# Kernel optimization log

Hardware: AMD Instinct MI355X
Metric: run time of the kernel (lower is better)

## Reference

```python
import jax, jax.numpy as jnp
import numpy as np
from jax import lax

STRIDE = 4
NSAMPLE = 16
EPS = 1e-5


def farthest_point_sample(xyz, npoint):
    # xyz: [B, N, 3] -> indices [B, npoint]. Deterministic start at index 0.
    B, N, _ = xyz.shape
    def step(carry, _):
        distance, farthest = carry
        centroid = jnp.take_along_axis(xyz, farthest[:, None, None], axis=1)  # [B,1,3]
        dist = jnp.sum((xyz - centroid) ** 2, axis=-1)  # [B,N]
        distance = jnp.minimum(distance, dist)
        new_farthest = jnp.argmax(distance, axis=-1).astype(jnp.int32)
        return (distance, new_farthest), farthest
    init = (jnp.full((B, N), 1e10, dtype=xyz.dtype), jnp.zeros((B,), dtype=jnp.int32))
    _, cents = lax.scan(step, init, None, length=npoint)  # [npoint, B]
    return cents.T  # [B, npoint]


def index_points(points, idx):
    # points: [B, N, C], idx: [B, ...] -> [B, ..., C]
    B = points.shape[0]
    C = points.shape[-1]
    flat = idx.reshape(B, -1)
    out = jnp.take_along_axis(points, flat[..., None], axis=1)
    return out.reshape(*idx.shape, C)


def square_distance(src, dst):
    # src: [B,N,3], dst: [B,M,3] -> [B,N,M]
    d = -2.0 * jnp.einsum('bnc,bmc->bnm', src, dst)
    d += jnp.sum(src ** 2, -1)[:, :, None]
    d += jnp.sum(dst ** 2, -1)[:, None, :]
    return d


def setup_inputs() -> dict:
    key = jax.random.key(0)
    k1, k2, k3 = jax.random.split(key, 3)
    B, N, C_in, C_out = 8, 8192, 128, 256
    xyz = jax.random.normal(k1, (B, N, 3), dtype=jnp.float32)
    features = jax.random.normal(k2, (B, N, C_in), dtype=jnp.float32)
    W = jax.random.normal(k3, (C_in + 3, C_out), dtype=jnp.float32) * 0.05
    gamma = jnp.ones((C_out,), dtype=jnp.float32)
    beta = jnp.zeros((C_out,), dtype=jnp.float32)
    return {"xyz": xyz, "features": features, "W": W, "gamma": gamma, "beta": beta}


def reference(xyz, features, W, gamma, beta):
    B, N, _ = xyz.shape
    npoint = N // STRIDE
    # farthest point sampling
    fps_idx = farthest_point_sample(xyz, npoint)               # [B, npoint]
    new_xyz = index_points(xyz, fps_idx)                       # [B, npoint, 3]
    # knn grouping
    dist = square_distance(new_xyz, xyz)                       # [B, npoint, N]
    _, idx = lax.top_k(-dist, NSAMPLE)                         # [B, npoint, k]
    grouped_xyz = index_points(xyz, idx)                       # [B, npoint, k, 3]
    grouped_xyz_norm = grouped_xyz - new_xyz[:, :, None]       # relative coords
    grouped_features = index_points(features, idx)             # [B, npoint, k, C]
    g = jnp.concatenate([grouped_xyz_norm, grouped_features], axis=-1)  # [B,np,k,3+C]
    # linear (no bias) -> BatchNorm2d (training-mode batch stats over B,np,k) -> relu
    h = jnp.einsum('bnkc,cd->bnkd', g, W)                      # [B,np,k,C_out]
    mean = jnp.mean(h, axis=(0, 1, 2))
    var = jnp.var(h, axis=(0, 1, 2))
    h = (h - mean) * lax.rsqrt(var + EPS) * gamma + beta
    h = jax.nn.relu(h)
    new_features = jnp.max(h, axis=2)                          # max over neighbors
    return (new_xyz, new_features)
```

## Files before the change

kernel.cpp:

```cpp
#include <hip/hip_runtime.h>

#define NPTS 8192
#define NP   2048
#define NB   8
#define CIN  128
#define COUT 256
#define KNN_K 16
#define GQ_TOTAL (NB * NP)
#define FB_GEMM_BLOCKS 512
#define FB_GEMM_QPB 32
#define CONS 248
#define NTICK 2048

typedef unsigned long long u64;
typedef float __attribute__((ext_vector_type(2))) f32x2;

__device__ __forceinline__ float mulrn(float a, float b){ return __fmul_rn(a,b); }
__device__ __forceinline__ float addrn(float a, float b){ return __fadd_rn(a,b); }
__device__ __forceinline__ float subrn(float a, float b){ return __fsub_rn(a,b); }

__device__ __forceinline__ void coh_store_f(float* p, float v) {
  __hip_atomic_store((int*)p, __float_as_int(v), __ATOMIC_RELAXED,
                     __HIP_MEMORY_SCOPE_AGENT);
}
__device__ __forceinline__ float coh_load_f(const float* p) {
  int v = __hip_atomic_load((const int*)p, __ATOMIC_RELAXED,
                            __HIP_MEMORY_SCOPE_AGENT);
  return __int_as_float(v);
}

struct FpsSm  { float4 p[NPTS]; u64 red[2][8]; };
struct ConsSm { float4 pts[NPTS]; float sg[2][16][132]; int sknn[8][16]; };
union  MegaSm { FpsSm f; ConsSm c; };

template <bool PUB>
__device__ __forceinline__ void fps_body(const float* __restrict__ base,
    float* __restrict__ outb, FpsSm& S, int* prog_b, const int tid) {
  const int lane = tid & 63;
  const int wid = tid >> 6;
  f32x2 px2[8], py2[8], pz2[8], dist2[8];
  const int i0 = tid * 16;
  {
    const float4* b4 = (const float4*)(base + (size_t)i0 * 3);
#pragma unroll
    for (int q = 0; q < 4; ++q) {
      float4 v0 = b4[q*3+0], v1 = b4[q*3+1], v2 = b4[q*3+2];
      px2[q*2+0] = f32x2{v0.x, v0.w};  py2[q*2+0] = f32x2{v0.y, v1.x};  pz2[q*2+0] = f32x2{v0.z, v1.y};
      px2[q*2+1] = f32x2{v1.z, v2.y};  py2[q*2+1] = f32x2{v1.w, v2.z};  pz2[q*2+1] = f32x2{v2.x, v2.w};
    }
  }
#pragma unroll
  for (int q = 0; q < 8; ++q) {
    S.p[i0 + 2*q + 0] = make_float4(px2[q].x, py2[q].x, pz2[q].x, 0.0f);
    S.p[i0 + 2*q + 1] = make_float4(px2[q].y, py2[q].y, pz2[q].y, 0.0f);
    dist2[q] = f32x2{1e10f, 1e10f};
  }
  if (tid == 0) {
    if (PUB) { coh_store_f(&outb[0], px2[0].x); coh_store_f(&outb[1], py2[0].x);
               coh_store_f(&outb[2], pz2[0].x); }
    else     { outb[0] = px2[0].x; outb[1] = py2[0].x; outb[2] = pz2[0].x; }
  }
  __syncthreads();
  float cx = S.p[0].x, cy = S.p[0].y, cz = S.p[0].z;

#pragma unroll 1
  for (int s = 1; s < NP; ++s) {
    const int p = s & 1;
    float bv = -1.0f; int bi = 0;
    {
#pragma clang fp contract(off)
      const f32x2 c2x = f32x2{cx, cx};
      const f32x2 c2y = f32x2{cy, cy};
      const f32x2 c2z = f32x2{cz, cz};
#pragma unroll
      for (int q = 0; q < 8; ++q) {
        f32x2 dx = px2[q] - c2x;
        f32x2 dy = py2[q] - c2y;
        f32x2 dz = pz2[q] - c2z;
        f32x2 xx = dx * dx;
        f32x2 yy = dy * dy;
        f32x2 zz = dz * dz;
        f32x2 ss = (xx + yy) + zz;
        float dm0 = fminf(dist2[q].x, ss.x);
        float dm1 = fminf(dist2[q].y, ss.y);
        dist2[q].x = dm0; dist2[q].y = dm1;
        bool g0 = dm0 > bv;
        bi = g0 ? (i0 + 2*q + 0) : bi;
        bv = g0 ? dm0 : bv;
        bool g1 = dm1 > bv;
        bi = g1 ? (i0 + 2*q + 1) : bi;
        bv = g1 ? dm1 : bv;
      }
    }
    u64 pk = ((u64)__float_as_uint(bv) << 32) | (unsigned)(8191 - bi);
#pragma unroll
    for (int off = 1; off < 64; off <<= 1) {
      u64 ov = __shfl_xor(pk, off, 64);
      pk = (ov > pk) ? ov : pk;
    }
    if (lane == 0) S.red[p][wid] = pk;
    __syncthreads();
    u64 t0=S.red[p][0], t1=S.red[p][1], t2=S.red[p][2], t3=S.red[p][3];
    u64 t4=S.red[p][4], t5=S.red[p][5], t6=S.red[p][6], t7=S.red[p][7];
    t0=(t1>t0)?t1:t0; t2=(t3>t2)?t3:t2; t4=(t5>t4)?t5:t4; t6=(t7>t6)?t7:t6;
    t0=(t2>t0)?t2:t0; t4=(t6>t4)?t6:t4;
    t0=(t4>t0)?t4:t0;
    const int ri = 8191 - (int)((unsigned)(t0 & 0xffffffffu));
    const float4 c = S.p[ri];
    cx = c.x; cy = c.y; cz = c.z;
    if (tid == 0) {
      const size_t o = (size_t)s * 3;
      if (PUB) {
        coh_store_f(&outb[o+0], cx); coh_store_f(&outb[o+1], cy);
        coh_store_f(&outb[o+2], cz);
        if ((s & 15) == 15) {
          asm volatile("s_waitcnt vmcnt(0)" ::: "memory");
          __hip_atomic_store(prog_b, s + 1, __ATOMIC_RELAXED,
                             __HIP_MEMORY_SCOPE_AGENT);
        }
      } else {
        outb[o+0]=cx; outb[o+1]=cy; outb[o+2]=cz;
      }
    }
  }
  if (PUB && tid == 0) {
    asm volatile("s_waitcnt vmcnt(0)" ::: "memory");
    __hip_atomic_store(prog_b, NP, __ATOMIC_RELAXED, __HIP_MEMORY_SCOPE_AGENT);
  }
}

__device__ __forceinline__ void knn_one(const float4* __restrict__ s_pts,
    const float qx, const float qy, const float qz, const int lane,
    int* __restrict__ gout, int* __restrict__ lout) {
  const float qn = addrn(addrn(mulrn(qx,qx), mulrn(qy,qy)), mulrn(qz,qz));
  float bd = (lane < 16) ? 1e30f : -1e30f;
  int   bi = 0;
  float r = 1e30f;
#pragma unroll 1
  for (int c0 = 0; c0 < NPTS; c0 += 64) {
    float4 p = s_pts[c0 + lane];
    float dot = addrn(addrn(mulrn(qx, p.x), mulrn(qy, p.y)), mulrn(qz, p.z));
    float dd = addrn(addrn(mulrn(-2.0f, dot), qn), p.w);
    u64 m = __ballot(dd < r);
    while (m) {
      int src = __builtin_ctzll(m);
      m &= (m - 1);
      float v = __shfl(dd, src, 64);
      if (v < r) {
        int vi = c0 + src;
        float bdn = __shfl_down(bd, 1, 64);
        int   bin_ = __shfl_down(bi, 1, 64);
        bool c1 = bdn > v;
        bool c2 = bd > v;
        float nb  = c1 ? bdn  : (c2 ? v  : bd);
        int   nbi = c1 ? bin_ : (c2 ? vi : bi);
        bd = (lane < 16) ? nb  : -1e30f;
        bi = (lane < 16) ? nbi : bi;
        r = __shfl(bd, 0, 64);
      }
    }
  }
  if (lane < 16) {
    if (gout) gout[lane] = bi;
    if (lout) lout[lane] = bi;
  }
}

__global__ __launch_bounds__(512) void k_mega(const float* __restrict__ xyz,
    const float* __restrict__ feat, const float* __restrict__ W,
    float* __restrict__ out_xyz, int* __restrict__ knn,
    float* __restrict__ part_sum, float* __restrict__ part_sq,
    float* __restrict__ hmax_buf, float* __restrict__ hmin_buf,
    int* __restrict__ prog) {
  __shared__ MegaSm sm;
  const int tid = threadIdx.x;
  if (blockIdx.x < NB) {
    const int b = blockIdx.x;
    fps_body<true>(xyz + (size_t)b * NPTS * 3, out_xyz + (size_t)b * NP * 3,
                   sm.f, &prog[b], tid);
    return;
  }
  const int c = blockIdx.x - NB;
  const int b = c & 7;
  ConsSm& S = sm.c;
  const float* base = xyz + (size_t)b * NPTS * 3;
  for (int i = tid; i < NPTS; i += 512) {
    float x = base[i*3+0], y = base[i*3+1], z = base[i*3+2];
    float n = addrn(addrn(mulrn(x,x), mulrn(y,y)), mulrn(z,z));
    S.pts[i] = make_float4(x, y, z, n);
  }
  const int d = tid & 255;
  const int h = tid >> 8;
  float w[132];
#pragma unroll
  for (int cc = 0; cc < 132; ++cc) {
    if (cc < 128)      w[cc] = W[(size_t)(3 + cc) * COUT + d];
    else if (cc < 131) w[cc] = W[(size_t)(cc - 128) * COUT + d];
    else               w[cc] = 0.0f;
  }
  float psum = 0.0f, psq = 0.0f;
  const int lane = tid & 63;
  const int wv = tid >> 6;
  __syncthreads();
#pragma unroll 1
  for (int t = c; t < NTICK; t += CONS) {
    const int g = t >> 3;
    const int need = g * 8 + 8;
    if (tid == 0) {
      while (__hip_atomic_load(&prog[b], __ATOMIC_RELAXED,
                               __HIP_MEMORY_SCOPE_AGENT) < need)
        __builtin_amdgcn_s_sleep(16);
    }
    __syncthreads();
    {
      const int gq = b * NP + g * 8 + wv;
      const float qx = coh_load_f(&out_xyz[(size_t)gq*3+0]);
      const float qy = coh_load_f(&out_xyz[(size_t)gq*3+1]);
      const float qz = coh_load_f(&out_xyz[(size_t)gq*3+2]);
      knn_one(S.pts, qx, qy, qz, lane, &knn[(size_t)gq * KNN_K], &S.sknn[wv][0]);
    }
    __syncthreads();
#pragma unroll 1
    for (int i = 0; i < 4; ++i) {
      const int ql = h * 4 + i;
      const int gq = b * NP + g * 8 + ql;
      {
        const int row = d >> 4, sub = d & 15;
        const int nidx = S.sknn[ql][row];
        const float* frow = feat + ((size_t)b * NPTS + nidx) * CIN;
        const float4 a0 = *(const float4*)(frow + sub * 8);
        const float4 a1 = *(const float4*)(frow + sub * 8 + 4);
        *(float4*)&S.sg[h][row][sub * 8]     = a0;
        *(float4*)&S.sg[h][row][sub * 8 + 4] = a1;
        if (sub == 0) {
          const float gx = xyz[((size_t)b * NPTS + nidx) * 3 + 0];
          const float gy = xyz[((size_t)b * NPTS + nidx) * 3 + 1];
          const float gz = xyz[((size_t)b * NPTS + nidx) * 3 + 2];
          const float qx = coh_load_f(&out_xyz[(size_t)gq*3+0]);
          const float qy = coh_load_f(&out_xyz[(size_t)gq*3+1]);
          const float qz = coh_load_f(&out_xyz[(size_t)gq*3+2]);
          *(float4*)&S.sg[h][row][128] = make_float4(gx-qx, gy-qy, gz-qz, 0.0f);
        }
      }
      __syncthreads();
      float hmax = -1e30f, hmin = 1e30f;
#pragma unroll 1
      for (int k = 0; k < 16; ++k) {
        float a0 = 0.f, a1 = 0.f, a2 = 0.f, a3 = 0.f;
#pragma unroll
        for (int c4 = 0; c4 < 33; ++c4) {
          float4 gg = *(const float4*)&S.sg[h][k][c4 * 4];
          a0 = fmaf(gg.x, w[c4 * 4 + 0], a0);
          a1 = fmaf(gg.y, w[c4 * 4 + 1], a1);
          a2 = fmaf(gg.z, w[c4 * 4 + 2], a2);
          a3 = fmaf(gg.w, w[c4 * 4 + 3], a3);
        }
        float hv = (a0 + a1) + (a2 + a3);
        psum += hv; psq = fmaf(hv, hv, psq);
        hmax = fmaxf(hmax, hv); hmin = fminf(hmin, hv);
      }
      hmax_buf[(size_t)gq * COUT + d] = hmax;
      hmin_buf[(size_t)gq * COUT + d] = hmin;
      __syncthreads();
    }
  }
  part_sum[((size_t)c * 2 + h) * COUT + d] = psum;
  part_sq [((size_t)c * 2 + h) * COUT + d] = psq;
}

__global__ void k_init(int* __restrict__ prog) {
  if (threadIdx.x < NB) prog[threadIdx.x] = 0;
}

__global__ __launch_bounds__(512) void k_fps(const float* __restrict__ xyz,
                                             float* __restrict__ out_xyz) {
  __shared__ FpsSm S;
  fps_body<false>(xyz + (size_t)blockIdx.x * NPTS * 3,
                  out_xyz + (size_t)blockIdx.x * NP * 3, S, nullptr, threadIdx.x);
}

__global__ __launch_bounds__(512) void k_knn(const float* __restrict__ xyz,
                                             const float* __restrict__ new_xyz,
                                             int* __restrict__ knn) {
  __shared__ float4 s_pts[NPTS];
  const int gq0 = blockIdx.x * 64;
  const int b = gq0 >> 11;
  const float* base = xyz + (size_t)b * NPTS * 3;
  for (int i = threadIdx.x; i < NPTS; i += 512) {
    float x = base[i*3+0], y = base[i*3+1], z = base[i*3+2];
    float n = addrn(addrn(mulrn(x,x), mulrn(y,y)), mulrn(z,z));
    s_pts[i] = make_float4(x, y, z, n);
  }
  __syncthreads();
  const int wave = threadIdx.x >> 6;
  const int lane = threadIdx.x & 63;
#pragma unroll 1
  for (int qi = 0; qi < 8; ++qi) {
    const int gq = gq0 + wave * 8 + qi;
    knn_one(s_pts, new_xyz[(size_t)gq*3+0], new_xyz[(size_t)gq*3+1],
            new_xyz[(size_t)gq*3+2], lane, &knn[(size_t)gq * KNN_K], nullptr);
  }
}

__global__ __launch_bounds__(256) void k_gemm(const float* __restrict__ feat,
    const float* __restrict__ xyz, const float* __restrict__ new_xyz,
    const int* __restrict__ knn, const float* __restrict__ W,
    float* __restrict__ part_sum, float* __restrict__ part_sq,
    float* __restrict__ hmax_buf, float* __restrict__ hmin_buf,
    const float* __restrict__ scale, const float* __restrict__ bias,
    float* __restrict__ out, int mode) {
  __shared__ float sg[16][132];
  const int d = threadIdx.x;
  float w[132];
#pragma unroll
  for (int c = 0; c < 132; ++c) {
    if (c < 128)      w[c] = W[(size_t)(3 + c) * COUT + d];
    else if (c < 131) w[c] = W[(size_t)(c - 128) * COUT + d];
    else              w[c] = 0.0f;
  }
  float psum = 0.0f, psq = 0.0f;
  float sc = 0.0f, bb = 0.0f;
  if (mode == 1) { sc = scale[d]; bb = bias[d]; }
#pragma unroll 1
  for (int i = 0; i < FB_GEMM_QPB; ++i) {
    const int gq = blockIdx.x * FB_GEMM_QPB + i;
    const int b = gq >> 11;
    {
      const int row = d >> 4, sub = d & 15;
      const int nidx = knn[(size_t)gq * KNN_K + row];
      const float* frow = feat + ((size_t)b * NPTS + nidx) * CIN;
      const float4 a0 = *(const float4*)(frow + sub * 8);
      const float4 a1 = *(const float4*)(frow + sub * 8 + 4);
      *(float4*)&sg[row][sub * 8]     = a0;
      *(float4*)&sg[row][sub * 8 + 4] = a1;
      if (sub == 0) {
        const float gx = xyz[((size_t)b * NPTS + nidx) * 3 + 0];
        const float gy = xyz[((size_t)b * NPTS + nidx) * 3 + 1];
        const float gz = xyz[((size_t)b * NPTS + nidx) * 3 + 2];
        const float qx = new_xyz[(size_t)gq * 3 + 0];
        const float qy = new_xyz[(size_t)gq * 3 + 1];
        const float qz = new_xyz[(size_t)gq * 3 + 2];
        *(float4*)&sg[row][128] = make_float4(gx - qx, gy - qy, gz - qz, 0.0f);
      }
    }
    __syncthreads();
    float hmax = -1e30f, hmin = 1e30f;
#pragma unroll 1
    for (int k = 0; k < 16; ++k) {
      float a0 = 0.f, a1 = 0.f, a2 = 0.f, a3 = 0.f;
#pragma unroll
      for (int c4 = 0; c4 < 33; ++c4) {
        float4 g = *(const float4*)&sg[k][c4 * 4];
        a0 = fmaf(g.x, w[c4 * 4 + 0], a0);
        a1 = fmaf(g.y, w[c4 * 4 + 1], a1);
        a2 = fmaf(g.z, w[c4 * 4 + 2], a2);
        a3 = fmaf(g.w, w[c4 * 4 + 3], a3);
      }
      float hv = (a0 + a1) + (a2 + a3);
      if (mode == 0) { psum += hv; psq = fmaf(hv, hv, psq); }
      hmax = fmaxf(hmax, hv); hmin = fminf(hmin, hv);
    }
    if (mode == 0) {
      if (hmax_buf) {
        hmax_buf[(size_t)gq * COUT + d] = hmax;
        hmin_buf[(size_t)gq * COUT + d] = hmin;
      }
    } else {
      float hsel = (sc >= 0.0f) ? hmax : hmin;
      out[(size_t)gq * COUT + d] = fmaxf(fmaf(sc, hsel, bb), 0.0f);
    }
    __syncthreads();
  }
  if (mode == 0) {
    part_sum[(size_t)blockIdx.x * COUT + d] = psum;
    part_sq [(size_t)blockIdx.x * COUT + d] = psq;
  }
}

__global__ __launch_bounds__(256) void k_stats(const float* __restrict__ part_sum,
    const float* __restrict__ part_sq, const float* __restrict__ gamma,
    const float* __restrict__ beta, float* __restrict__ scale,
    float* __restrict__ bias, int nrows) {
  const int d = threadIdx.x;
  float s = 0.0f, q = 0.0f;
  for (int bl = 0; bl < nrows; ++bl) {
    s += part_sum[(size_t)bl * COUT + d];
    q += part_sq[(size_t)bl * COUT + d];
  }
  const float inv = 1.0f / 262144.0f;
  float mean = s * inv;
  float var = q * inv - mean * mean;
  float scv = gamma[d] / sqrtf(var + 1e-5f);
  scale[d] = scv;
  bias[d] = beta[d] - mean * scv;
}

__global__ __launch_bounds__(256) void k_final(const float* __restrict__ hmax_buf,
    const float* __restrict__ hmin_buf, const float* __restrict__ scale,
    const float* __restrict__ bias, float* __restrict__ out) {
  const int e4 = (blockIdx.x * 256 + threadIdx.x) * 4;
  const int d0 = e4 & (COUT - 1);
  const float4 hx = *(const float4*)&hmax_buf[e4];
  const float4 hn = *(const float4*)&hmin_buf[e4];
  const float4 sc = *(const float4*)&scale[d0];
  const float4 bb = *(const float4*)&bias[d0];
  float4 o;
  o.x = fmaxf(fmaf(sc.x, (sc.x >= 0.f) ? hx.x : hn.x, bb.x), 0.f);
  o.y = fmaxf(fmaf(sc.y, (sc.y >= 0.f) ? hx.y : hn.y, bb.y), 0.f);
  o.z = fmaxf(fmaf(sc.z, (sc.z >= 0.f) ? hx.z : hn.z, bb.z), 0.f);
  o.w = fmaxf(fmaf(sc.w, (sc.w >= 0.f) ? hx.w : hn.w, bb.w), 0.f);
  *(float4*)&out[e4] = o;
}

extern "C" void kernel_launch(void* const* d_in, const int* in_sizes, int n_in,
                              void* d_out, int out_size, void* d_ws, size_t ws_size,
                              hipStream_t stream) {
  const float* xyz   = (const float*)d_in[0];
  const float* feat  = (const float*)d_in[1];
  const float* W     = (const float*)d_in[2];
  const float* gamma = (const float*)d_in[3];
  const float* beta  = (const float*)d_in[4];
  float* out_xyz = (float*)d_out;
  float* out_nf  = out_xyz + (size_t)NB * NP * 3;

  char* ws = (char*)d_ws;
  int*   knn      = (int*)ws;
  float* hmax_buf = (float*)(ws + (1 << 20));
  float* hmin_buf = (float*)(ws + (1 << 20) + (size_t)GQ_TOTAL*COUT*4);
  char*  ws3      = ws + (1 << 20) + 2ull * GQ_TOTAL * COUT * 4;
  float* part_sum = (float*)ws3;
  float* part_sq  = (float*)(ws3 + (size_t)FB_GEMM_BLOCKS * COUT * 4);
  int*   prog     = (int*)(ws3 + 2ull * FB_GEMM_BLOCKS * COUT * 4);
  float* scale    = (float*)((char*)prog + 64);
  float* bias     = scale + COUT;
  const size_t need = (1ull << 20) + 2ull * GQ_TOTAL * COUT * 4
                    + 2ull * FB_GEMM_BLOCKS * COUT * 4 + 64 + 2 * COUT * 4;

  bool mega_ok = false;
  if (ws_size >= need) {
    hipLaunchKernelGGL(k_init, dim3(1), dim3(64), 0, stream, prog);
    void* args[] = {(void*)&xyz, (void*)&feat, (void*)&W, (void*)&out_xyz,
                    (void*)&knn, (void*)&part_sum, (void*)&part_sq,
                    (void*)&hmax_buf, (void*)&hmin_buf, (void*)&prog};
    hipError_t e = hipLaunchCooperativeKernel((const void*)k_mega, dim3(NB + CONS),
                                              dim3(512), args, 0, stream);
    if (e == hipSuccess) {
      hipLaunchKernelGGL(k_stats, dim3(1), dim3(256), 0, stream, part_sum, part_sq,
                         gamma, beta, scale, bias, CONS * 2);
      hipLaunchKernelGGL(k_final, dim3(GQ_TOTAL * COUT / 1024), dim3(256), 0,
                         stream, hmax_buf, hmin_buf, scale, bias, out_nf);
      mega_ok = true;
    }
  }
  if (!mega_ok) {
    hipLaunchKernelGGL(k_fps, dim3(NB), dim3(512), 0, stream, xyz, out_xyz);
    hipLaunchKernelGGL(k_knn, dim3(256), dim3(512), 0, stream, xyz, out_xyz, knn);
    if (ws_size >= need) {
      hipLaunchKernelGGL(k_gemm, dim3(FB_GEMM_BLOCKS), dim3(256), 0, stream, feat,
                         xyz, out_xyz, knn, W, part_sum, part_sq, hmax_buf,
                         hmin_buf, (const float*)nullptr, (const float*)nullptr,
                         (float*)nullptr, 0);
      hipLaunchKernelGGL(k_stats, dim3(1), dim3(256), 0, stream, part_sum, part_sq,
                         gamma, beta, scale, bias, FB_GEMM_BLOCKS);
      hipLaunchKernelGGL(k_final, dim3(GQ_TOTAL * COUT / 1024), dim3(256), 0,
                         stream, hmax_buf, hmin_buf, scale, bias, out_nf);
    } else {
      float* f_ps = (float*)(ws + (1 << 20));
      float* f_pq = f_ps + FB_GEMM_BLOCKS * COUT;
      float* f_sc = f_pq + FB_GEMM_BLOCKS * COUT;
      float* f_bb = f_sc + COUT;
      hipLaunchKernelGGL(k_gemm, dim3(FB_GEMM_BLOCKS), dim3(256), 0, stream, feat,
                         xyz, out_xyz, knn, W, f_ps, f_pq, (float*)nullptr,
                         (float*)nullptr, (const float*)nullptr,
                         (const float*)nullptr, (float*)nullptr, 0);
      hipLaunchKernelGGL(k_stats, dim3(1), dim3(256), 0, stream, f_ps, f_pq,
                         gamma, beta, f_sc, f_bb, FB_GEMM_BLOCKS);
      hipLaunchKernelGGL(k_gemm, dim3(FB_GEMM_BLOCKS), dim3(256), 0, stream, feat,
                         xyz, out_xyz, knn, W, (float*)nullptr, (float*)nullptr,
                         (float*)nullptr, (float*)nullptr, f_sc, f_bb, out_nf, 1);
    }
  }
}
```

Baseline: 2.317 ms.

## Fuse BN stats and finalize into mega kernel, use DPP wave reduction

Folds the batch-norm statistics reduction and the final scale/bias/ReLU pass into the cooperative mega kernel. Blocks publish their partial sums and bump a counter; block 0 reduces the partials and publishes scale and bias, and every block then finalizes its slice of outputs. This removes two extra kernel launches and their gaps. It also replaces the shuffle-based argmax reduction in FPS with DPP row and broadcast operations, and publishes FPS progress every 8 samples instead of every 16, at the cost of spin-waits and more frequent atomic stores.

```diff
diff --git a/kernel.cpp b/kernel.cpp
--- a/kernel.cpp
+++ b/kernel.cpp
@@ -27,6 +27,18 @@
   int v = __hip_atomic_load((const int*)p, __ATOMIC_RELAXED,
                             __HIP_MEMORY_SCOPE_AGENT);
   return __int_as_float(v);
+}
+
+template <int CTRL>
+__device__ __forceinline__ u64 dpp_max_u64(u64 pk) {
+  int lo = __builtin_amdgcn_update_dpp((int)(unsigned)(pk & 0xffffffffu),
+                                       (int)(unsigned)(pk & 0xffffffffu),
+                                       CTRL, 0xf, 0xf, false);
+  int hi = __builtin_amdgcn_update_dpp((int)(unsigned)(pk >> 32),
+                                       (int)(unsigned)(pk >> 32),
+                                       CTRL, 0xf, 0xf, false);
+  u64 o = ((u64)(unsigned)hi << 32) | (unsigned)lo;
+  return (o > pk) ? o : pk;
 }
 
 struct FpsSm  { float4 p[NPTS]; u64 red[2][8]; };
@@ -93,12 +105,13 @@
       }
     }
     u64 pk = ((u64)__float_as_uint(bv) << 32) | (unsigned)(8191 - bi);
-#pragma unroll
-    for (int off = 1; off < 64; off <<= 1) {
-      u64 ov = __shfl_xor(pk, off, 64);
-      pk = (ov > pk) ? ov : pk;
-    }
-    if (lane == 0) S.red[p][wid] = pk;
+    pk = dpp_max_u64<0x111>(pk);
+    pk = dpp_max_u64<0x112>(pk);
+    pk = dpp_max_u64<0x114>(pk);
+    pk = dpp_max_u64<0x118>(pk);
+    pk = dpp_max_u64<0x142>(pk);
+    pk = dpp_max_u64<0x143>(pk);
+    if (lane == 63) S.red[p][wid] = pk;
     __syncthreads();
     u64 t0=S.red[p][0], t1=S.red[p][1], t2=S.red[p][2], t3=S.red[p][3];
     u64 t4=S.red[p][4], t5=S.red[p][5], t6=S.red[p][6], t7=S.red[p][7];
@@ -113,7 +126,7 @@
       if (PUB) {
         coh_store_f(&outb[o+0], cx); coh_store_f(&outb[o+1], cy);
         coh_store_f(&outb[o+2], cz);
-        if ((s & 15) == 15) {
+        if ((s & 7) == 7) {
           asm volatile("s_waitcnt vmcnt(0)" ::: "memory");
           __hip_atomic_store(prog_b, s + 1, __ATOMIC_RELAXED,
                              __HIP_MEMORY_SCOPE_AGENT);
@@ -168,9 +181,12 @@
 
 __global__ __launch_bounds__(512) void k_mega(const float* __restrict__ xyz,
     const float* __restrict__ feat, const float* __restrict__ W,
-    float* __restrict__ out_xyz, int* __restrict__ knn,
+    const float* __restrict__ gamma, const float* __restrict__ beta,
+    float* __restrict__ out_xyz, float* __restrict__ out_nf,
+    int* __restrict__ knn,
     float* __restrict__ part_sum, float* __restrict__ part_sq,
     float* __restrict__ hmax_buf, float* __restrict__ hmin_buf,
+    float* __restrict__ scale, float* __restrict__ bias,
     int* __restrict__ prog) {
   __shared__ MegaSm sm;
   const int tid = threadIdx.x;
@@ -264,12 +280,64 @@
       __syncthreads();
     }
   }
-  part_sum[((size_t)c * 2 + h) * COUT + d] = psum;
-  part_sq [((size_t)c * 2 + h) * COUT + d] = psq;
+  coh_store_f(&part_sum[((size_t)c * 2 + h) * COUT + d], psum);
+  coh_store_f(&part_sq [((size_t)c * 2 + h) * COUT + d], psq);
+  asm volatile("s_waitcnt vmcnt(0)" ::: "memory");
+  __syncthreads();
+  if (tid == 0)
+    __hip_atomic_fetch_add(&prog[8], 1, __ATOMIC_RELAXED,
+                           __HIP_MEMORY_SCOPE_AGENT);
+  if (c == 0) {
+    if (tid == 0) {
+      while (__hip_atomic_load(&prog[8], __ATOMIC_RELAXED,
+                               __HIP_MEMORY_SCOPE_AGENT) < CONS)
+        __builtin_amdgcn_s_sleep(16);
+    }
+    __syncthreads();
+    if (tid < 256) {
+      float s = 0.0f, q = 0.0f;
+#pragma unroll 1
+      for (int r = 0; r < CONS * 2; ++r) {
+        s += coh_load_f(&part_sum[(size_t)r * COUT + tid]);
+        q += coh_load_f(&part_sq [(size_t)r * COUT + tid]);
+      }
+      const float inv = 1.0f / 262144.0f;
+      float mean = s * inv;
+      float var = q * inv - mean * mean;
+      float scv = gamma[tid] / sqrtf(var + 1e-5f);
+      coh_store_f(&scale[tid], scv);
+      coh_store_f(&bias[tid], beta[tid] - mean * scv);
+    }
+    asm volatile("s_waitcnt vmcnt(0)" ::: "memory");
+    __syncthreads();
+    if (tid == 0)
+      __hip_atomic_store(&prog[9], 1, __ATOMIC_RELAXED,
+                         __HIP_MEMORY_SCOPE_AGENT);
+  }
+  if (tid == 0) {
+    while (__hip_atomic_load(&prog[9], __ATOMIC_RELAXED,
+                             __HIP_MEMORY_SCOPE_AGENT) < 1)
+      __builtin_amdgcn_s_sleep(16);
+  }
+  __syncthreads();
+  const float sc = coh_load_f(&scale[d]);
+  const float bb = coh_load_f(&bias[d]);
+#pragma unroll 1
+  for (int t = c; t < NTICK; t += CONS) {
+    const int g = t >> 3;
+#pragma unroll
+    for (int i = 0; i < 4; ++i) {
+      const int gq = b * NP + g * 8 + h * 4 + i;
+      const float hx = hmax_buf[(size_t)gq * COUT + d];
+      const float hn = hmin_buf[(size_t)gq * COUT + d];
+      const float hsel = (sc >= 0.0f) ? hx : hn;
+      out_nf[(size_t)gq * COUT + d] = fmaxf(fmaf(sc, hsel, bb), 0.0f);
+    }
+  }
 }
 
 __global__ void k_init(int* __restrict__ prog) {
-  if (threadIdx.x < NB) prog[threadIdx.x] = 0;
+  if (threadIdx.x < 16) prog[threadIdx.x] = 0;
 }
 
 __global__ __launch_bounds__(512) void k_fps(const float* __restrict__ xyz,
@@ -439,18 +507,15 @@
   bool mega_ok = false;
   if (ws_size >= need) {
     hipLaunchKernelGGL(k_init, dim3(1), dim3(64), 0, stream, prog);
-    void* args[] = {(void*)&xyz, (void*)&feat, (void*)&W, (void*)&out_xyz,
-                    (void*)&knn, (void*)&part_sum, (void*)&part_sq,
-                    (void*)&hmax_buf, (void*)&hmin_buf, (void*)&prog};
+    void* args[] = {(void*)&xyz, (void*)&feat, (void*)&W,
+                    (void*)&gamma, (void*)&beta,
+                    (void*)&out_xyz, (void*)&out_nf, (void*)&knn,
+                    (void*)&part_sum, (void*)&part_sq,
+                    (void*)&hmax_buf, (void*)&hmin_buf,
+                    (void*)&scale, (void*)&bias, (void*)&prog};
     hipError_t e = hipLaunchCooperativeKernel((const void*)k_mega, dim3(NB + CONS),
                                               dim3(512), args, 0, stream);
-    if (e == hipSuccess) {
-      hipLaunchKernelGGL(k_stats, dim3(1), dim3(256), 0, stream, part_sum, part_sq,
-                         gamma, beta, scale, bias, CONS * 2);
-      hipLaunchKernelGGL(k_final, dim3(GQ_TOTAL * COUT / 1024), dim3(256), 0,
-                         stream, hmax_buf, hmin_buf, scale, bias, out_nf);
-      mega_ok = true;
-    }
+    mega_ok = (e == hipSuccess);
   }
   if (!mega_ok) {
     hipLaunchKernelGGL(k_fps, dim3(NB), dim3(512), 0, stream, xyz, out_xyz);
```

After: 2.096 ms (median of 2 runs). 9.6% less time.
